# Optimization experiments

Hardware: AMD Instinct MI355X
Metric: run time of the kernel (lower is better)

## Reference

```python
import jax, jax.numpy as jnp
import numpy as np

N_HEADS = 16

def setup_inputs() -> dict:
    key = jax.random.key(0)
    ks = jax.random.split(key, 5)
    B, N, D = 2, 2048, 1024
    return {
        "x": jax.random.normal(ks[0], (B, N, D), dtype=jnp.float32),
        "w_qkv": jax.random.normal(ks[1], (D, 3 * D), dtype=jnp.float32) * (1.0 / np.sqrt(D)),
        "b_qkv": jax.random.normal(ks[2], (3 * D,), dtype=jnp.float32) * 0.02,
        "w_out": jax.random.normal(ks[3], (D, D), dtype=jnp.float32) * (1.0 / np.sqrt(D)),
        "b_out": jax.random.normal(ks[4], (D,), dtype=jnp.float32) * 0.02,
    }

def reference(x, w_qkv, b_qkv, w_out, b_out):
    B, N, D = x.shape
    H = N_HEADS
    dk = D // H
    qkv = x @ w_qkv + b_qkv                       # (B, N, 3D)
    # NOTE: original reshapes to (B, N, H, 3*dk) then chunks -> per-head interleaved layout
    qkv = qkv.reshape(B, N, H, 3 * dk).transpose(2, 0, 1, 3)  # (H, B, N, 3*dk)
    q, k, v = jnp.split(qkv, 3, axis=-1)          # each (H, B, N, dk)
    scale = 1.0 / np.sqrt(dk).astype(np.float32)
    scores = jnp.einsum('hbnd,hbmd->hbnm', q, k) * scale  # (H, B, N, N)
    attn = jax.nn.softmax(scores, axis=-1)
    context = jnp.einsum('hbnm,hbmd->hbnd', attn, v)       # (H, B, N, dk)
    context = context.transpose(1, 2, 0, 3).reshape(B, N, D)
    attn_mean = attn.mean(axis=0).mean(axis=1)    # (B, N): mean over heads then over query dim
    out = context @ w_out + b_out
    return out, attn_mean
```

## Files before the change

### kernel.cpp

```cpp
#include <hip/hip_runtime.h>
#include <hip/hip_bf16.h>
#include <stdint.h>

#define B_ 2
#define N_ 2048
#define D_ 1024
#define H_ 16
#define DK 64

typedef __bf16 bf16x8 __attribute__((ext_vector_type(8)));
typedef short s16x4 __attribute__((ext_vector_type(4)));
typedef float f32x4 __attribute__((ext_vector_type(4)));

#define EXP2SC 0.18033688011112042f

__device__ __forceinline__ unsigned short f2bf(float f) {
    unsigned int u = __float_as_uint(f);
    u = (u + 0x7FFFu + ((u >> 16) & 1u)) >> 16;
    return (unsigned short)u;
}

__device__ __forceinline__ short2 pkbf(float a, float b) {
    __hip_bfloat162 t = __float22bfloat162_rn(float2{a, b});
    return *(short2*)&t;
}

__device__ __forceinline__ void glds16(const void* g, void* l) {
    __builtin_amdgcn_global_load_lds(
        (const __attribute__((address_space(1))) void*)g,
        (__attribute__((address_space(3))) void*)l, 16, 0, 0);
}

__global__ __launch_bounds__(256) void k_prep(const float* __restrict__ x,
                                              unsigned short* __restrict__ xb,
                                              const float* __restrict__ w_qkv,
                                              unsigned short* __restrict__ wqkvT,
                                              const float* __restrict__ w_out,
                                              unsigned short* __restrict__ woutT,
                                              float* __restrict__ amean) {
    __shared__ float tile[32][33];
    int blk = blockIdx.x, t = threadIdx.x;
    if (blk < 1024) {
        const float4* x4 = (const float4*)x;
        ushort4* o4 = (ushort4*)xb;
        int i = blk * 256 + t;
#pragma unroll
        for (int s = 0; s < 4; ++s, i += 262144) {
            float4 v = x4[i];
            ushort4 o;
            o.x = f2bf(v.x); o.y = f2bf(v.y); o.z = f2bf(v.z); o.w = f2bf(v.w);
            o4[i] = o;
        }
    } else if (blk < 4096) {
        int idx = blk - 1024;
        int c0 = (idx % 96) * 32, k0 = (idx / 96) * 32;
        int tx = t & 31, ty = t >> 5;
        for (int s = 0; s < 4; ++s)
            tile[ty + 8 * s][tx] = w_qkv[(size_t)(k0 + ty + 8 * s) * 3072 + c0 + tx];
        __syncthreads();
        for (int s = 0; s < 4; ++s)
            wqkvT[(size_t)(c0 + ty + 8 * s) * 1024 + k0 + tx] = f2bf(tile[tx][ty + 8 * s]);
    } else if (blk < 5120) {
        int idx = blk - 4096;
        int c0 = (idx % 32) * 32, k0 = (idx / 32) * 32;
        int tx = t & 31, ty = t >> 5;
        for (int s = 0; s < 4; ++s)
            tile[ty + 8 * s][tx] = w_out[(size_t)(k0 + ty + 8 * s) * 1024 + c0 + tx];
        __syncthreads();
        for (int s = 0; s < 4; ++s)
            woutT[(size_t)(c0 + ty + 8 * s) * 1024 + k0 + tx] = f2bf(tile[tx][ty + 8 * s]);
    } else {
#pragma unroll
        for (int s = 0; s < 16; ++s) amean[s * 256 + t] = 0.f;
    }
}

__global__ __launch_bounds__(256) void k_gemm_qkv(const unsigned short* __restrict__ A,
                                                  const unsigned short* __restrict__ BT,
                                                  const float* __restrict__ bias,
                                                  unsigned short* __restrict__ Cout,
                                                  int M, int Nn, int K) {
    __shared__ __attribute__((aligned(16))) unsigned short Alds[128 * 64];
    __shared__ __attribute__((aligned(16))) unsigned short Blds[128 * 64];
    int t = threadIdx.x;
    int lane = t & 63, w = t >> 6;
    int quad = lane >> 4, c = lane & 15;
    int wm = w >> 1, wn = w & 1;
    int bi = blockIdx.y, bj = blockIdx.x;
    const unsigned short* Abase = A + (size_t)(bi * 128) * K;
    const unsigned short* Bbase = BT + (size_t)(bj * 128) * K;

    f32x4 acc[4][4];
#pragma unroll
    for (int mf = 0; mf < 4; ++mf)
#pragma unroll
        for (int nf = 0; nf < 4; ++nf)
            acc[mf][nf] = (f32x4){0.f, 0.f, 0.f, 0.f};

    for (int k0 = 0; k0 < K; k0 += 64) {
        __syncthreads();
#pragma unroll
        for (int i = 0; i < 4; ++i) {
            int ch = i * 256 + t;
            int row = ch >> 3, kc = (ch & 7) ^ (row & 7);
            glds16(&Abase[(size_t)row * K + k0 + kc * 8], (char*)Alds + ch * 16);
            glds16(&Bbase[(size_t)row * K + k0 + kc * 8], (char*)Blds + ch * 16);
        }
        __syncthreads();
#pragma unroll
        for (int ks = 0; ks < 2; ++ks) {
            bf16x8 af[4], bfr[4];
#pragma unroll
            for (int mf = 0; mf < 4; ++mf)
                af[mf] = *(const bf16x8*)&Alds[(wm * 64 + mf * 16 + c) * 64 +
                                               (((ks * 4 + quad) ^ (c & 7)) * 8)];
#pragma unroll
            for (int nf = 0; nf < 4; ++nf)
                bfr[nf] = *(const bf16x8*)&Blds[(wn * 64 + nf * 16 + c) * 64 +
                                                (((ks * 4 + quad) ^ (c & 7)) * 8)];
#pragma unroll
            for (int mf = 0; mf < 4; ++mf)
#pragma unroll
                for (int nf = 0; nf < 4; ++nf)
                    acc[mf][nf] = __builtin_amdgcn_mfma_f32_16x16x32_bf16(af[mf], bfr[nf],
                                                                          acc[mf][nf], 0, 0, 0);
        }
    }

#pragma unroll
    for (int mf = 0; mf < 4; ++mf)
#pragma unroll
        for (int nf = 0; nf < 4; ++nf) {
            int j = bj * 128 + wn * 64 + nf * 16 + c;
            float bv = bias[j];
            int h = j / 192, r2 = j % 192;
            int which = r2 >> 6, d = r2 & 63;
#pragma unroll
            for (int r = 0; r < 4; ++r) {
                int i = bi * 128 + wm * 64 + mf * 16 + quad * 4 + r;
                float v = acc[mf][nf][r] + bv;
                if (which == 0) v *= EXP2SC;
                int b = i >> 11, n = i & 2047;
                size_t dst;
                if (which < 2)
                    dst = (size_t)which * 4194304 + (((size_t)(h * 2 + b) * 2048 + n) * 64 + d);
                else
                    dst = (size_t)2 * 4194304 + (((size_t)(h * 2 + b) * 64 + d) * 2048 + n);
                Cout[dst] = f2bf(v);
            }
        }
}

__global__ __launch_bounds__(256) void k_gemm_out(const unsigned short* __restrict__ A,
                                                  const unsigned short* __restrict__ BT,
                                                  const float* __restrict__ bias,
                                                  float* __restrict__ C,
                                                  int M, int Nn, int K) {
    __shared__ __attribute__((aligned(16))) unsigned short Alds[64 * 64];
    __shared__ __attribute__((aligned(16))) unsigned short Blds[128 * 64];
    int t = threadIdx.x;
    int lane = t & 63, w = t >> 6;
    int quad = lane >> 4, c = lane & 15;
    int wm = w >> 1, wn = w & 1;
    int bi = blockIdx.y, bj = blockIdx.x;
    const unsigned short* Abase = A + (size_t)(bi * 64) * K;
    const unsigned short* Bbase = BT + (size_t)(bj * 128) * K;

    f32x4 acc[2][4];
#pragma unroll
    for (int mf = 0; mf < 2; ++mf)
#pragma unroll
        for (int nf = 0; nf < 4; ++nf)
            acc[mf][nf] = (f32x4){0.f, 0.f, 0.f, 0.f};

    for (int k0 = 0; k0 < K; k0 += 64) {
        __syncthreads();
#pragma unroll
        for (int i = 0; i < 2; ++i) {
            int ch = i * 256 + t;
            int row = ch >> 3, kc = (ch & 7) ^ (row & 7);
            glds16(&Abase[(size_t)row * K + k0 + kc * 8], (char*)Alds + ch * 16);
        }
#pragma unroll
        for (int i = 0; i < 4; ++i) {
            int ch = i * 256 + t;
            int row = ch >> 3, kc = (ch & 7) ^ (row & 7);
            glds16(&Bbase[(size_t)row * K + k0 + kc * 8], (char*)Blds + ch * 16);
        }
        __syncthreads();
#pragma unroll
        for (int ks = 0; ks < 2; ++ks) {
            bf16x8 af[2], bfr[4];
#pragma unroll
            for (int mf = 0; mf < 2; ++mf)
                af[mf] = *(const bf16x8*)&Alds[(wm * 32 + mf * 16 + c) * 64 +
                                               (((ks * 4 + quad) ^ (c & 7)) * 8)];
#pragma unroll
            for (int nf = 0; nf < 4; ++nf)
                bfr[nf] = *(const bf16x8*)&Blds[(wn * 64 + nf * 16 + c) * 64 +
                                                (((ks * 4 + quad) ^ (c & 7)) * 8)];
#pragma unroll
            for (int mf = 0; mf < 2; ++mf)
#pragma unroll
                for (int nf = 0; nf < 4; ++nf)
                    acc[mf][nf] = __builtin_amdgcn_mfma_f32_16x16x32_bf16(af[mf], bfr[nf],
                                                                          acc[mf][nf], 0, 0, 0);
        }
    }

#pragma unroll
    for (int mf = 0; mf < 2; ++mf)
#pragma unroll
        for (int nf = 0; nf < 4; ++nf) {
            int j = bj * 128 + wn * 64 + nf * 16 + c;
            float bv = bias[j];
#pragma unroll
            for (int r = 0; r < 4; ++r) {
                int i = bi * 64 + wm * 32 + mf * 16 + quad * 4 + r;
                C[(size_t)i * Nn + j] = acc[mf][nf][r] + bv;
            }
        }
}

__global__ __launch_bounds__(512) void k_attn(const unsigned short* __restrict__ Q,
                                              const unsigned short* __restrict__ Kc,
                                              const unsigned short* __restrict__ VT,
                                              unsigned short* __restrict__ ctx,
                                              float* __restrict__ lrs_out) {
    __shared__ __attribute__((aligned(16))) unsigned short lds[16384];
    int t = threadIdx.x, lane = t & 63, w = t >> 6;
    int quad = lane >> 4, c = lane & 15;
    int bi = blockIdx.x;
    int hb = bi & 31, qt = bi >> 5;
    int h = hb >> 1, b = hb & 1;
    const unsigned short* qbase = Q + (size_t)hb * 131072 + (size_t)(qt * 256 + w * 32) * 64;
    const unsigned short* kbase = Kc + (size_t)hb * 131072;
    const unsigned short* vtbase = VT + (size_t)hb * 131072;

    int srow = t >> 3, sB = t & 7;
    int sgoff = srow * 64 + ((sB ^ (srow & 7)) * 8);
    int vgoff = srow * 2048 + ((sB ^ (srow & 7)) * 8);

    bf16x8 qf[2][2];
#pragma unroll
    for (int qs = 0; qs < 2; ++qs)
#pragma unroll
        for (int ks = 0; ks < 2; ++ks)
            qf[qs][ks] = *(const bf16x8*)&qbase[(qs * 16 + c) * 64 + ks * 32 + quad * 8];

    glds16(&kbase[sgoff], (char*)lds + t * 16);
    glds16(&vtbase[vgoff], (char*)(lds + 4096) + t * 16);

    f32x4 acc[2][4];
#pragma unroll
    for (int qs = 0; qs < 2; ++qs)
#pragma unroll
        for (int ds = 0; ds < 4; ++ds) acc[qs][ds] = (f32x4){0.f, 0.f, 0.f, 0.f};
    float lsum[2] = {0.f, 0.f};

    for (int kb = 0; kb < 32; ++kb) {
        const unsigned short* Kb = lds + (kb & 1) * 8192;
        const unsigned short* Vb = Kb + 4096;
        __syncthreads();
        if (kb < 31) {
            unsigned short* Kn = lds + ((kb + 1) & 1) * 8192;
            glds16(&kbase[(size_t)(kb + 1) * 4096 + sgoff], (char*)Kn + t * 16);
            glds16(&vtbase[(size_t)(kb + 1) * 64 + vgoff], (char*)(Kn + 4096) + t * 16);
        }

        f32x4 st[4][2];
#pragma unroll
        for (int ksub = 0; ksub < 4; ++ksub)
#pragma unroll
            for (int qs = 0; qs < 2; ++qs) st[ksub][qs] = (f32x4){0.f, 0.f, 0.f, 0.f};
#pragma unroll
        for (int ks = 0; ks < 2; ++ks)
#pragma unroll
            for (int ksub = 0; ksub < 4; ++ksub) {
                bf16x8 kf = *(const bf16x8*)&Kb[(ksub * 16 + c) * 64 +
                                                (((ks * 4 + quad) ^ (c & 7)) * 8)];
#pragma unroll
                for (int qs = 0; qs < 2; ++qs)
                    st[ksub][qs] =
                        __builtin_amdgcn_mfma_f32_16x16x32_bf16(kf, qf[qs][ks], st[ksub][qs],
                                                                0, 0, 0);
            }
#pragma unroll
        for (int ksub = 0; ksub < 4; ++ksub) {
            s16x4 pf[2];
#pragma unroll
            for (int qs = 0; qs < 2; ++qs) {
                float p0 = __builtin_amdgcn_exp2f(st[ksub][qs][0]);
                float p1 = __builtin_amdgcn_exp2f(st[ksub][qs][1]);
                float p2 = __builtin_amdgcn_exp2f(st[ksub][qs][2]);
                float p3 = __builtin_amdgcn_exp2f(st[ksub][qs][3]);
                lsum[qs] += (p0 + p1) + (p2 + p3);
                short2 lo = pkbf(p0, p1), hi = pkbf(p2, p3);
                pf[qs] = (s16x4){lo.x, lo.y, hi.x, hi.y};
            }
            s16x4 vf[4];
#pragma unroll
            for (int ds = 0; ds < 4; ++ds) {
                int row = ds * 16 + c;
                vf[ds] = *(const s16x4*)&Vb[row * 64 +
                                            (((2 * ksub + (quad >> 1)) ^ (row & 7)) * 8) +
                                            (quad & 1) * 4];
            }
#pragma unroll
            for (int qs = 0; qs < 2; ++qs)
#pragma unroll
                for (int ds = 0; ds < 4; ++ds)
                    acc[qs][ds] = __builtin_amdgcn_mfma_f32_16x16x16bf16_1k(pf[qs], vf[ds],
                                                                            acc[qs][ds], 0, 0, 0);
        }
    }

#pragma unroll
    for (int qs = 0; qs < 2; ++qs) {
        float v = lsum[qs];
        v += __shfl_xor(v, 16);
        v += __shfl_xor(v, 32);
        if (lane < 16)
            lrs_out[hb * 2048 + qt * 256 + w * 32 + qs * 16 + c] =
                -(__builtin_amdgcn_logf(v) + 15.0f);
        float linv = 1.0f / v;
        float ir[4];
#pragma unroll
        for (int r = 0; r < 4; ++r) ir[r] = __shfl(linv, quad * 4 + r);
#pragma unroll
        for (int ds = 0; ds < 4; ++ds)
#pragma unroll
            for (int r = 0; r < 4; ++r) {
                int n = qt * 256 + w * 32 + qs * 16 + quad * 4 + r;
                ctx[((size_t)(b * 2048 + n)) * 1024 + h * 64 + ds * 16 + c] =
                    f2bf(acc[qs][ds][r] * ir[r]);
            }
    }
}

__global__ __launch_bounds__(512) void k_amean(const unsigned short* __restrict__ Q,
                                               const unsigned short* __restrict__ Kc,
                                               const float* __restrict__ lrs,
                                               float* __restrict__ amean) {
    __shared__ __attribute__((aligned(16))) unsigned short Qlds[16384];
    __shared__ float rslds[2][128];
    int t = threadIdx.x, lane = t & 63, w = t >> 6;
    int quad = lane >> 4, c = lane & 15;
    int bi = blockIdx.x;
    int hb = bi & 31, kt = bi >> 5, b = hb & 1;
    const unsigned short* kbase = Kc + (size_t)hb * 131072 + (size_t)(kt * 256 + w * 32) * 64;
    const unsigned short* qbase = Q + (size_t)hb * 131072;

    bf16x8 kf[2][2];
#pragma unroll
    for (int ksub = 0; ksub < 2; ++ksub)
#pragma unroll
        for (int ks = 0; ks < 2; ++ks)
            kf[ksub][ks] = *(const bf16x8*)&kbase[(ksub * 16 + c) * 64 + ks * 32 + quad * 8];

#pragma unroll
    for (int i = 0; i < 2; ++i) {
        int ch = i * 512 + t;
        int row = ch >> 3, Bs = ch & 7;
        glds16(&qbase[row * 64 + ((Bs ^ (row & 7)) * 8)], (char*)Qlds + ch * 16);
    }
    if (t < 128) rslds[0][t] = lrs[hb * 2048 + t];

    f32x4 colacc[2];
    colacc[0] = (f32x4){0.f, 0.f, 0.f, 0.f};
    colacc[1] = (f32x4){0.f, 0.f, 0.f, 0.f};

    for (int qc = 0; qc < 16; ++qc) {
        const unsigned short* Qb = Qlds + (qc & 1) * 8192;
        __syncthreads();
        if (qc < 15) {
            unsigned short* Qn = Qlds + ((qc + 1) & 1) * 8192;
#pragma unroll
            for (int i = 0; i < 2; ++i) {
                int ch = i * 512 + t;
                int row = ch >> 3, Bs = ch & 7;
                glds16(&qbase[(size_t)(qc + 1) * 8192 + row * 64 + ((Bs ^ (row & 7)) * 8)],
                       (char*)Qn + ch * 16);
            }
            if (t < 128) rslds[(qc + 1) & 1][t] = lrs[hb * 2048 + (qc + 1) * 128 + t];
        }
#pragma unroll
        for (int qs = 0; qs < 8; ++qs) {
            f32x4 st[2];
            st[0] = (f32x4){0.f, 0.f, 0.f, 0.f};
            st[1] = (f32x4){0.f, 0.f, 0.f, 0.f};
#pragma unroll
            for (int ks = 0; ks < 2; ++ks) {
                bf16x8 qfr = *(const bf16x8*)&Qb[(qs * 16 + c) * 64 +
                                                 (((ks * 4 + quad) ^ (c & 7)) * 8)];
#pragma unroll
                for (int ksub = 0; ksub < 2; ++ksub)
                    st[ksub] = __builtin_amdgcn_mfma_f32_16x16x32_bf16(kf[ksub][ks], qfr,
                                                                       st[ksub], 0, 0, 0);
            }
            float rv = rslds[qc & 1][qs * 16 + c];
#pragma unroll
            for (int ksub = 0; ksub < 2; ++ksub)
#pragma unroll
                for (int r = 0; r < 4; ++r)
                    colacc[ksub][r] += __builtin_amdgcn_exp2f(st[ksub][r] + rv);
        }
    }
#pragma unroll
    for (int ksub = 0; ksub < 2; ++ksub)
#pragma unroll
        for (int r = 0; r < 4; ++r) {
            float v = colacc[ksub][r];
            v += __shfl_xor(v, 1);
            v += __shfl_xor(v, 2);
            v += __shfl_xor(v, 4);
            v += __shfl_xor(v, 8);
            if (c == 0)
                atomicAdd(&amean[b * 2048 + kt * 256 + w * 32 + ksub * 16 + quad * 4 + r], v);
        }
}

extern "C" void kernel_launch(void* const* d_in, const int* in_sizes, int n_in,
                              void* d_out, int out_size, void* d_ws, size_t ws_size,
                              hipStream_t stream) {
    const float* x = (const float*)d_in[0];
    const float* w_qkv = (const float*)d_in[1];
    const float* b_qkv = (const float*)d_in[2];
    const float* w_out = (const float*)d_in[3];
    const float* b_out = (const float*)d_in[4];
    float* out = (float*)d_out;
    float* amean = out + 4194304;

    unsigned short* ws = (unsigned short*)d_ws;
    unsigned short* x_bf = ws;
    unsigned short* wqkvT = x_bf + 4194304;
    unsigned short* woutT = wqkvT + 3145728;
    unsigned short* q_bf = woutT + 1048576;
    unsigned short* k_bf = q_bf + 4194304;
    unsigned short* vT_bf = k_bf + 4194304;
    unsigned short* ctx_bf = vT_bf + 4194304;
    float* lrs = (float*)(ctx_bf + 4194304);

    k_prep<<<5121, 256, 0, stream>>>(x, x_bf, w_qkv, wqkvT, w_out, woutT, amean);
    k_gemm_qkv<<<dim3(24, 32), 256, 0, stream>>>(x_bf, wqkvT, b_qkv, q_bf, 4096, 3072, 1024);
    k_attn<<<256, 512, 0, stream>>>(q_bf, k_bf, vT_bf, ctx_bf, lrs);
    k_amean<<<256, 512, 0, stream>>>(q_bf, k_bf, lrs, amean);
    k_gemm_out<<<dim3(8, 64), 256, 0, stream>>>(ctx_bf, woutT, b_out, out, 4096, 1024, 1024);
}
```

Measured before the change: 221.6 us.

## Double-buffer LDS tiles in QKV and output projection GEMMs

Both projection GEMMs now use two LDS buffers. The next K-slice is issued with async global-to-LDS loads right after the barrier, while MFMAs work on the current slice. This replaces the old two-barriers-per-iteration load-then-compute pattern with one barrier per iteration, aiming to hide global load latency. In exchange, per-block LDS doubles (64 KB for the QKV GEMM), which may reduce occupancy. The loop count is hard-coded to K=1024. The compiler may also insert conservative waits on in-flight LDS DMA, which would limit the overlap.

Measured after the change: 208.8 us. 5.8% less time.

```diff
diff --git a/kernel.cpp b/kernel.cpp
--- a/kernel.cpp
+++ b/kernel.cpp
@@ -80,8 +80,7 @@
                                                   const float* __restrict__ bias,
                                                   unsigned short* __restrict__ Cout,
                                                   int M, int Nn, int K) {
-    __shared__ __attribute__((aligned(16))) unsigned short Alds[128 * 64];
-    __shared__ __attribute__((aligned(16))) unsigned short Blds[128 * 64];
+    __shared__ __attribute__((aligned(16))) unsigned short lds[32768];
     int t = threadIdx.x;
     int lane = t & 63, w = t >> 6;
     int quad = lane >> 4, c = lane & 15;
@@ -97,27 +96,35 @@
         for (int nf = 0; nf < 4; ++nf)
             acc[mf][nf] = (f32x4){0.f, 0.f, 0.f, 0.f};
 
-    for (int k0 = 0; k0 < K; k0 += 64) {
-        __syncthreads();
+    auto stage = [&](int k0, int p) {
+        unsigned short* Ab = lds + p * 16384;
+        unsigned short* Bb = Ab + 8192;
 #pragma unroll
         for (int i = 0; i < 4; ++i) {
             int ch = i * 256 + t;
             int row = ch >> 3, kc = (ch & 7) ^ (row & 7);
-            glds16(&Abase[(size_t)row * K + k0 + kc * 8], (char*)Alds + ch * 16);
-            glds16(&Bbase[(size_t)row * K + k0 + kc * 8], (char*)Blds + ch * 16);
-        }
-        __syncthreads();
+            glds16(&Abase[(size_t)row * K + k0 + kc * 8], (char*)Ab + ch * 16);
+            glds16(&Bbase[(size_t)row * K + k0 + kc * 8], (char*)Bb + ch * 16);
+        }
+    };
+    stage(0, 0);
+
+    for (int kb = 0; kb < 16; ++kb) {
+        __syncthreads();
+        if (kb < 15) stage((kb + 1) * 64, (kb + 1) & 1);
+        const unsigned short* Ab = lds + (kb & 1) * 16384;
+        const unsigned short* Bb = Ab + 8192;
 #pragma unroll
         for (int ks = 0; ks < 2; ++ks) {
             bf16x8 af[4], bfr[4];
 #pragma unroll
             for (int mf = 0; mf < 4; ++mf)
-                af[mf] = *(const bf16x8*)&Alds[(wm * 64 + mf * 16 + c) * 64 +
-                                               (((ks * 4 + quad) ^ (c & 7)) * 8)];
+                af[mf] = *(const bf16x8*)&Ab[(wm * 64 + mf * 16 + c) * 64 +
+                                             (((ks * 4 + quad) ^ (c & 7)) * 8)];
 #pragma unroll
             for (int nf = 0; nf < 4; ++nf)
-                bfr[nf] = *(const bf16x8*)&Blds[(wn * 64 + nf * 16 + c) * 64 +
-                                                (((ks * 4 + quad) ^ (c & 7)) * 8)];
+                bfr[nf] = *(const bf16x8*)&Bb[(wn * 64 + nf * 16 + c) * 64 +
+                                              (((ks * 4 + quad) ^ (c & 7)) * 8)];
 #pragma unroll
             for (int mf = 0; mf < 4; ++mf)
 #pragma unroll
@@ -156,8 +163,7 @@
                                                   const float* __restrict__ bias,
                                                   float* __restrict__ C,
                                                   int M, int Nn, int K) {
-    __shared__ __attribute__((aligned(16))) unsigned short Alds[64 * 64];
-    __shared__ __attribute__((aligned(16))) unsigned short Blds[128 * 64];
+    __shared__ __attribute__((aligned(16))) unsigned short lds[24576];
     int t = threadIdx.x;
     int lane = t & 63, w = t >> 6;
     int quad = lane >> 4, c = lane & 15;
@@ -173,32 +179,40 @@
         for (int nf = 0; nf < 4; ++nf)
             acc[mf][nf] = (f32x4){0.f, 0.f, 0.f, 0.f};
 
-    for (int k0 = 0; k0 < K; k0 += 64) {
-        __syncthreads();
+    auto stage = [&](int k0, int p) {
+        unsigned short* Ab = lds + p * 12288;
+        unsigned short* Bb = Ab + 4096;
 #pragma unroll
         for (int i = 0; i < 2; ++i) {
             int ch = i * 256 + t;
             int row = ch >> 3, kc = (ch & 7) ^ (row & 7);
-            glds16(&Abase[(size_t)row * K + k0 + kc * 8], (char*)Alds + ch * 16);
+            glds16(&Abase[(size_t)row * K + k0 + kc * 8], (char*)Ab + ch * 16);
         }
 #pragma unroll
         for (int i = 0; i < 4; ++i) {
             int ch = i * 256 + t;
             int row = ch >> 3, kc = (ch & 7) ^ (row & 7);
-            glds16(&Bbase[(size_t)row * K + k0 + kc * 8], (char*)Blds + ch * 16);
-        }
-        __syncthreads();
+            glds16(&Bbase[(size_t)row * K + k0 + kc * 8], (char*)Bb + ch * 16);
+        }
+    };
+    stage(0, 0);
+
+    for (int kb = 0; kb < 16; ++kb) {
+        __syncthreads();
+        if (kb < 15) stage((kb + 1) * 64, (kb + 1) & 1);
+        const unsigned short* Ab = lds + (kb & 1) * 12288;
+        const unsigned short* Bb = Ab + 4096;
 #pragma unroll
         for (int ks = 0; ks < 2; ++ks) {
             bf16x8 af[2], bfr[4];
 #pragma unroll
             for (int mf = 0; mf < 2; ++mf)
-                af[mf] = *(const bf16x8*)&Alds[(wm * 32 + mf * 16 + c) * 64 +
-                                               (((ks * 4 + quad) ^ (c & 7)) * 8)];
+                af[mf] = *(const bf16x8*)&Ab[(wm * 32 + mf * 16 + c) * 64 +
+                                             (((ks * 4 + quad) ^ (c & 7)) * 8)];
 #pragma unroll
             for (int nf = 0; nf < 4; ++nf)
-                bfr[nf] = *(const bf16x8*)&Blds[(wn * 64 + nf * 16 + c) * 64 +
-                                                (((ks * 4 + quad) ^ (c & 7)) * 8)];
+                bfr[nf] = *(const bf16x8*)&Bb[(wn * 64 + nf * 16 + c) * 64 +
+                                              (((ks * 4 + quad) ^ (c & 7)) * 8)];
 #pragma unroll
             for (int mf = 0; mf < 2; ++mf)
 #pragma unroll
```
